# Kernel optimization log

Hardware: AMD Instinct MI355X
Metric: run time of the kernel (lower is better)

Reference implementation:

```python
import jax, jax.numpy as jnp
import numpy as np

NEG_BIG = -2.0**32 + 1.0  # matches torch masked_fill value


def setup_inputs() -> dict:
    key = jax.random.key(0)
    ks = jax.random.split(key, 5)
    B, H, L, D = 8, 4, 256, 32
    return {
        "Q": jax.random.normal(ks[0], (B, H, L, D), jnp.float32),
        "K": jax.random.normal(ks[1], (B, H, L, D), jnp.float32),
        "V": jax.random.normal(ks[2], (B, H, L, D), jnp.float32),
        "time_matrix_K": jax.random.normal(ks[3], (B, H, L, L, D), jnp.float32),
        "time_matrix_V": jax.random.normal(ks[4], (B, H, L, L, D), jnp.float32),
        "attn_mask": jnp.zeros((L, L), jnp.float32),
        "padding_mask": jnp.zeros((B, L), bool),
    }


def reference(Q, K, V, time_matrix_K, time_matrix_V, attn_mask, padding_mask):
    scale = jnp.sqrt(jnp.asarray(Q.shape[-1], Q.dtype))
    # QK^T plus per-(q,k) time bias: tmK[b,h,q,k,:] . Q[b,h,q,:]
    energy = jnp.einsum("bhqd,bhkd->bhqk", Q, K)
    energy = energy + jnp.einsum("bhqkd,bhqd->bhqk", time_matrix_K, Q)
    energy = energy / scale
    energy = energy + attn_mask[None, None, :, :]  # additive mask
    energy = jnp.where(padding_mask[:, None, None, :], NEG_BIG, energy)
    attn = jax.nn.softmax(energy, axis=-1)  # [B,H,Lq,Lk]
    # attn @ V plus time-value contribution attn[b,h,q,:] . tmV[b,h,q,:,:]
    x = jnp.einsum("bhqk,bhkd->bhqd", attn, V)
    x = x + jnp.einsum("bhqk,bhqkd->bhqd", attn, time_matrix_V)
    return (x, attn)
```

## Files before the change

### kernel.cpp

```cpp
#include <hip/hip_runtime.h>
#include <math.h>


#define LDIM 256
#define DDIM 32
#define NEG_BIG (-4294967295.0f)

__global__ __launch_bounds__(256, 4)
void taspda_fused(const float* __restrict__ Q,
                  const float* __restrict__ K,
                  const float* __restrict__ V,
                  const float* __restrict__ tmK,
                  const float* __restrict__ tmV,
                  const float* __restrict__ attn_mask,
                  const unsigned char* __restrict__ padding_mask,
                  float* __restrict__ x_out,
                  float* __restrict__ attn_out)
{
    const int bid = blockIdx.x;
    const int q   = bid & (LDIM - 1);
    const int bh  = bid >> 8;
    const int b   = bh >> 2;
    const int t   = threadIdx.x;
    const int kk  = t >> 3;
    const int d4  = t & 7;

    __shared__ float  qlds[DDIM];
    __shared__ float  els[LDIM];
    __shared__ float  red[8];
    __shared__ float4 xred[256];

    if (t < DDIM) qlds[t] = Q[(size_t)bid * DDIM + t];
    __syncthreads();
    const float4 q4 = *(const float4*)&qlds[d4 * 4];

    const float4* tmKrow = (const float4*)(tmK + (size_t)bid * LDIM * DDIM);
    const float4* Krow   = (const float4*)(K   + (size_t)bh  * LDIM * DDIM);

    #pragma unroll
    for (int i = 0; i < 8; ++i) {
        const int k = kk + 32 * i;
        const float4 a = tmKrow[k * 8 + d4];
        const float4 c = Krow[k * 8 + d4];
        float s = q4.x * (a.x + c.x) + q4.y * (a.y + c.y)
                + q4.z * (a.z + c.z) + q4.w * (a.w + c.w);
        s += __shfl_xor(s, 1);
        s += __shfl_xor(s, 2);
        s += __shfl_xor(s, 4);
        if (d4 == 0) els[k] = s;
    }
    __syncthreads();

    const float inv_scale = 0.17677669529663687f;
    float e = els[t] * inv_scale + attn_mask[q * LDIM + t];
    if (padding_mask[b * LDIM + t]) e = NEG_BIG;

    float m = e;
    #pragma unroll
    for (int o = 32; o >= 1; o >>= 1) m = fmaxf(m, __shfl_xor(m, o));
    const int wid = t >> 6;
    if ((t & 63) == 0) red[wid] = m;
    __syncthreads();
    m = fmaxf(fmaxf(red[0], red[1]), fmaxf(red[2], red[3]));

    const float p = expf(e - m);
    float s = p;
    #pragma unroll
    for (int o = 32; o >= 1; o >>= 1) s += __shfl_xor(s, o);
    if ((t & 63) == 0) red[4 + wid] = s;
    __syncthreads();
    s = red[4] + red[5] + red[6] + red[7];
    const float attnv = p / s;

    attn_out[(size_t)bid * LDIM + t] = attnv;
    els[t] = attnv;
    __syncthreads();

    const float4* tmVrow = (const float4*)(tmV + (size_t)bid * LDIM * DDIM);
    const float4* Vrow   = (const float4*)(V   + (size_t)bh  * LDIM * DDIM);
    float4 acc = make_float4(0.f, 0.f, 0.f, 0.f);
    #pragma unroll
    for (int i = 0; i < 8; ++i) {
        const int k = kk + 32 * i;
        const float  a  = els[k];
        const float4 v  = Vrow[k * 8 + d4];
        const float4 tv = tmVrow[k * 8 + d4];
        acc.x += a * (v.x + tv.x);
        acc.y += a * (v.y + tv.y);
        acc.z += a * (v.z + tv.z);
        acc.w += a * (v.w + tv.w);
    }
    xred[t] = acc;
    __syncthreads();
    #pragma unroll
    for (int o = 128; o >= 8; o >>= 1) {
        if (t < o) {
            float4 other = xred[t + o];
            float4 mine  = xred[t];
            mine.x += other.x; mine.y += other.y;
            mine.z += other.z; mine.w += other.w;
            xred[t] = mine;
        }
        __syncthreads();
    }
    if (t < 8) {
        ((float4*)(x_out + (size_t)bid * DDIM))[t] = xred[t];
    }
}

extern "C" void kernel_launch(void* const* d_in, const int* in_sizes, int n_in,
                              void* d_out, int out_size, void* d_ws, size_t ws_size,
                              hipStream_t stream) {
    const float* Q   = (const float*)d_in[0];
    const float* K   = (const float*)d_in[1];
    const float* V   = (const float*)d_in[2];
    const float* tmK = (const float*)d_in[3];
    const float* tmV = (const float*)d_in[4];
    const float* am  = (const float*)d_in[5];
    const unsigned char* pm = (const unsigned char*)d_in[6];

    float* x_out    = (float*)d_out;
    float* attn_out = x_out + (size_t)8 * 4 * 256 * 32;

    const int blocks = 8 * 4 * 256;
    taspda_fused<<<blocks, 256, 0, stream>>>(Q, K, V, tmK, tmV, am, pm, x_out, attn_out);
}
```

Measured before the change: 514.4 us.

## Prefetch tmV/V before softmax, use nontemporal streams, shuffle-based reductions

Issues the tmV and V loads into registers before the softmax barrier so the second large stream overlaps the softmax phase. Streaming tensors now use nontemporal loads and stores. The softmax is merged into one barrier using per-wave max/sum with rescaling and fast exp. The LDS tree reduction of the output is replaced by wave shuffles plus a small 4-way combine. Holding 16 extra float4 values per thread raises register pressure and may reduce occupancy.

```diff
diff --git a/kernel.cpp b/kernel.cpp
--- a/kernel.cpp
+++ b/kernel.cpp
@@ -1,6 +1,8 @@
 #include <hip/hip_runtime.h>
 #include <math.h>
 
+
+typedef float v4f __attribute__((ext_vector_type(4)));
 
 #define LDIM 256
 #define DDIM 32
@@ -24,24 +26,24 @@
     const int t   = threadIdx.x;
     const int kk  = t >> 3;
     const int d4  = t & 7;
+    const int wid = t >> 6;
 
-    __shared__ float  qlds[DDIM];
-    __shared__ float  els[LDIM];
-    __shared__ float  red[8];
-    __shared__ float4 xred[256];
+    __shared__ float els[LDIM];
+    __shared__ float red[8];
+    __shared__ v4f   xpart[4][8];
 
-    if (t < DDIM) qlds[t] = Q[(size_t)bid * DDIM + t];
-    __syncthreads();
-    const float4 q4 = *(const float4*)&qlds[d4 * 4];
+    const v4f q4 = *(const v4f*)(Q + (size_t)bid * DDIM + d4 * 4);
 
-    const float4* tmKrow = (const float4*)(tmK + (size_t)bid * LDIM * DDIM);
-    const float4* Krow   = (const float4*)(K   + (size_t)bh  * LDIM * DDIM);
+    const v4f* tmKrow = (const v4f*)(tmK + (size_t)bid * (LDIM * DDIM));
+    const v4f* Krow   = (const v4f*)(K   + (size_t)bh  * (LDIM * DDIM));
+    const v4f* tmVrow = (const v4f*)(tmV + (size_t)bid * (LDIM * DDIM));
+    const v4f* Vrow   = (const v4f*)(V   + (size_t)bh  * (LDIM * DDIM));
 
     #pragma unroll
     for (int i = 0; i < 8; ++i) {
         const int k = kk + 32 * i;
-        const float4 a = tmKrow[k * 8 + d4];
-        const float4 c = Krow[k * 8 + d4];
+        v4f a = __builtin_nontemporal_load(tmKrow + k * 8 + d4);
+        v4f c = Krow[k * 8 + d4];
         float s = q4.x * (a.x + c.x) + q4.y * (a.y + c.y)
                 + q4.z * (a.z + c.z) + q4.w * (a.w + c.w);
         s += __shfl_xor(s, 1);
@@ -49,62 +51,59 @@
         s += __shfl_xor(s, 4);
         if (d4 == 0) els[k] = s;
     }
+
+    v4f tv[8], vv[8];
+    #pragma unroll
+    for (int i = 0; i < 8; ++i) {
+        const int k = kk + 32 * i;
+        tv[i] = __builtin_nontemporal_load(tmVrow + k * 8 + d4);
+        vv[i] = Vrow[k * 8 + d4];
+    }
+
     __syncthreads();
 
     const float inv_scale = 0.17677669529663687f;
     float e = els[t] * inv_scale + attn_mask[q * LDIM + t];
     if (padding_mask[b * LDIM + t]) e = NEG_BIG;
 
-    float m = e;
+    float mw = e;
     #pragma unroll
-    for (int o = 32; o >= 1; o >>= 1) m = fmaxf(m, __shfl_xor(m, o));
-    const int wid = t >> 6;
-    if ((t & 63) == 0) red[wid] = m;
+    for (int o = 32; o >= 1; o >>= 1) mw = fmaxf(mw, __shfl_xor(mw, o));
+    const float p = __expf(e - mw);
+    float sw = p;
+    #pragma unroll
+    for (int o = 32; o >= 1; o >>= 1) sw += __shfl_xor(sw, o);
+    if ((t & 63) == 0) { red[wid] = mw; red[4 + wid] = sw; }
     __syncthreads();
-    m = fmaxf(fmaxf(red[0], red[1]), fmaxf(red[2], red[3]));
 
-    const float p = expf(e - m);
-    float s = p;
-    #pragma unroll
-    for (int o = 32; o >= 1; o >>= 1) s += __shfl_xor(s, o);
-    if ((t & 63) == 0) red[4 + wid] = s;
-    __syncthreads();
-    s = red[4] + red[5] + red[6] + red[7];
-    const float attnv = p / s;
+    const float m = fmaxf(fmaxf(red[0], red[1]), fmaxf(red[2], red[3]));
+    const float s = red[4] * __expf(red[0] - m) + red[5] * __expf(red[1] - m)
+                  + red[6] * __expf(red[2] - m) + red[7] * __expf(red[3] - m);
+    const float attnv = p * __expf(mw - m) / s;
 
-    attn_out[(size_t)bid * LDIM + t] = attnv;
+    __builtin_nontemporal_store(attnv, attn_out + (size_t)bid * LDIM + t);
     els[t] = attnv;
     __syncthreads();
 
-    const float4* tmVrow = (const float4*)(tmV + (size_t)bid * LDIM * DDIM);
-    const float4* Vrow   = (const float4*)(V   + (size_t)bh  * LDIM * DDIM);
-    float4 acc = make_float4(0.f, 0.f, 0.f, 0.f);
+    v4f acc = {0.f, 0.f, 0.f, 0.f};
     #pragma unroll
     for (int i = 0; i < 8; ++i) {
         const int k = kk + 32 * i;
-        const float  a  = els[k];
-        const float4 v  = Vrow[k * 8 + d4];
-        const float4 tv = tmVrow[k * 8 + d4];
-        acc.x += a * (v.x + tv.x);
-        acc.y += a * (v.y + tv.y);
-        acc.z += a * (v.z + tv.z);
-        acc.w += a * (v.w + tv.w);
+        const float a = els[k];
+        acc += a * (vv[i] + tv[i]);
     }
-    xred[t] = acc;
+    #pragma unroll
+    for (int o = 8; o <= 32; o <<= 1) {
+        acc.x += __shfl_xor(acc.x, o);
+        acc.y += __shfl_xor(acc.y, o);
+        acc.z += __shfl_xor(acc.z, o);
+        acc.w += __shfl_xor(acc.w, o);
+    }
+    if ((t & 63) < 8) xpart[wid][d4] = acc;
     __syncthreads();
-    #pragma unroll
-    for (int o = 128; o >= 8; o >>= 1) {
-        if (t < o) {
-            float4 other = xred[t + o];
-            float4 mine  = xred[t];
-            mine.x += other.x; mine.y += other.y;
-            mine.z += other.z; mine.w += other.w;
-            xred[t] = mine;
-        }
-        __syncthreads();
-    }
     if (t < 8) {
-        ((float4*)(x_out + (size_t)bid * DDIM))[t] = xred[t];
+        v4f r = xpart[0][t] + xpart[1][t] + xpart[2][t] + xpart[3][t];
+        __builtin_nontemporal_store(r, (v4f*)(x_out + (size_t)bid * DDIM) + t);
     }
 }
 
```

Result: no change. 506.0 us (-1.6%).
